# Kernel optimization log

Hardware: AMD Instinct MI355X
Metric: run time of the kernel (lower is better)

Reference implementation:

```python
import jax, jax.numpy as jnp
import numpy as np

B, Q, DIN, DOUT = 1, 1024, 4096, 4096
H, G, HD = 32, 8, 128          # heads, kv groups, head_dim; group_size = H // G
PREV = 3072                     # cached KV length
MAXPOS = 4096                   # rope table length (>= PREV + Q)
START = PREV


def _rope_tables(max_pos, head_dim):
    half = head_dim // 2
    inv_freq = 1.0 / (10000.0 ** (jnp.arange(half, dtype=jnp.float32) / half))
    ang = jnp.arange(max_pos, dtype=jnp.float32)[:, None] * inv_freq[None, :]
    ang = jnp.concatenate([ang, ang], axis=-1)  # [max_pos, head_dim]
    return jnp.cos(ang), jnp.sin(ang)


def apply_rope(x, cos, sin, start_pos):
    # x: [b, h, s, d]; rotate-half RoPE with absolute positions start_pos..start_pos+s
    s, d = x.shape[2], x.shape[3]
    c = cos[start_pos:start_pos + s]  # [s, d] (start_pos is a Python int)
    sn = sin[start_pos:start_pos + s]
    x1, x2 = x[..., : d // 2], x[..., d // 2:]
    rotated = jnp.concatenate([-x2, x1], axis=-1)
    return x * c + rotated * sn


def setup_inputs() -> dict:
    key = jax.random.key(0)
    ks = jax.random.split(key, 7)
    x = jax.random.normal(ks[0], (B, Q, DIN), dtype=jnp.float32)
    cos, sin = _rope_tables(MAXPOS, HD)
    # causal mask: query at abs position START+i may attend kv position j <= START+i
    qpos = START + jnp.arange(Q)
    kpos = jnp.arange(START + Q)
    mask = (kpos[None, :] > qpos[:, None])[None, None]  # [1,1,Q,KV], True = masked
    prev_k = jax.random.normal(ks[1], (B, G, PREV, HD), dtype=jnp.float32)
    prev_v = jax.random.normal(ks[2], (B, G, PREV, HD), dtype=jnp.float32)
    sc = 0.02
    Wq = jax.random.normal(ks[3], (DIN, DOUT), dtype=jnp.float32) * sc
    Wk = jax.random.normal(ks[4], (DIN, G * HD), dtype=jnp.float32) * sc
    Wv = jax.random.normal(ks[5], (DIN, G * HD), dtype=jnp.float32) * sc
    Wo = jax.random.normal(ks[6], (DOUT, DOUT), dtype=jnp.float32) * sc
    return dict(x=x, mask=mask, cos=cos, sin=sin, start_pos=START,
                prev_k=prev_k, prev_v=prev_v, Wq=Wq, Wk=Wk, Wv=Wv, Wo=Wo)


def reference(x, mask, cos, sin, start_pos, prev_k, prev_v, Wq, Wk, Wv, Wo):
    b, s, _ = x.shape
    gs = H // G  # group_size
    q = (x @ Wq).reshape(b, s, H, HD).transpose(0, 2, 1, 3)   # [b,H,s,hd]
    k = (x @ Wk).reshape(b, s, G, HD).transpose(0, 2, 1, 3)   # [b,G,s,hd]
    v = (x @ Wv).reshape(b, s, G, HD).transpose(0, 2, 1, 3)
    q = apply_rope(q, cos, sin, start_pos)
    k = apply_rope(k, cos, sin, start_pos)
    keys = jnp.concatenate([prev_k, k], axis=2)    # [b,G,KV,hd]
    values = jnp.concatenate([prev_v, v], axis=2)
    # grouped attention (equivalent to repeat_interleave of K/V over group_size)
    qg = q.reshape(b, G, gs, s, HD)
    scores = jnp.einsum('bgnqd,bgkd->bgnqk', qg, keys)        # [b,G,gs,s,KV]
    scores = jnp.where(mask[:, :, None], -jnp.inf, scores)
    attn = jax.nn.softmax(scores / np.sqrt(HD).astype(np.float32), axis=-1)
    ctx = jnp.einsum('bgnqk,bgkd->bgnqd', attn, values)       # [b,G,gs,s,hd]
    ctx = ctx.reshape(b, H, s, HD).transpose(0, 2, 1, 3).reshape(b, s, DOUT)
    out = ctx @ Wo
    return (out, keys, values)
```

## Files before the change

kernel.cpp:

```cpp
#include <hip/hip_runtime.h>
#include <hip/hip_bf16.h>

typedef unsigned short u16;
typedef unsigned int u32;
typedef __attribute__((ext_vector_type(4))) float f32x4;
typedef __attribute__((ext_vector_type(16))) float f32x16;
typedef __attribute__((ext_vector_type(8))) __bf16 bf16x8;
typedef __attribute__((ext_vector_type(4))) u16 u16x4;
typedef __attribute__((ext_vector_type(8))) u16 u16x8;
typedef __attribute__((ext_vector_type(4))) u32 u32x4;

#define START_POS 3072
#define NKV 4096
#define HD_ 128
#define SEQ 1024
#define DIN_ 4096
#define DQKV 6144

__device__ __forceinline__ void gll16(const void* g, void* l) {
  __builtin_amdgcn_global_load_lds((const __attribute__((address_space(1))) u32*)g,
                                   (__attribute__((address_space(3))) u32*)l, 16, 0, 0);
}
__device__ __forceinline__ u16 f2bf(float f) {
  u32 u = __builtin_bit_cast(u32, f);
  return (u16)((u + 0x7fffu + ((u >> 16) & 1u)) >> 16);
}
__device__ __forceinline__ u32 pack2bf(float a, float b) {
  __hip_bfloat162 t = __float22bfloat162_rn(float2{a, b});
  u32 u; __builtin_memcpy(&u, &t, 4);
  return u;
}
__device__ __forceinline__ f32x4 mfma16(bf16x8 a, bf16x8 b, f32x4 c) {
  return __builtin_amdgcn_mfma_f32_16x16x32_bf16(a, b, c, 0, 0, 0);
}
__device__ __forceinline__ f32x16 mfma32(bf16x8 a, bf16x8 b, f32x16 c) {
  return __builtin_amdgcn_mfma_f32_32x32x16_bf16(a, b, c, 0, 0, 0);
}

__global__ __launch_bounds__(256) void wtrans(const float* __restrict__ W,
    u16* __restrict__ Wt, int N, int ntn, int row_off)
{
  __shared__ float T[64][68];
  int bid = blockIdx.x;
  int nt = bid % ntn, kt = bid / ntn;
  int t = threadIdx.x;
  int kl = t >> 4, nl4 = (t & 15) << 2;
#pragma unroll
  for (int r = 0; r < 4; r++) {
    int row = r * 16 + kl;
    f32x4 v = *(const f32x4*)(W + (size_t)(kt * 64 + row) * N + nt * 64 + nl4);
    T[row][nl4] = v[0]; T[row][nl4 + 1] = v[1]; T[row][nl4 + 2] = v[2]; T[row][nl4 + 3] = v[3];
  }
  __syncthreads();
  int nl = t >> 2, k0 = (t & 3) << 4;
  u16x8 lo, hi;
#pragma unroll
  for (int j = 0; j < 8; j++) lo[j] = f2bf(T[k0 + j][nl]);
#pragma unroll
  for (int j = 0; j < 8; j++) hi[j] = f2bf(T[k0 + 8 + j][nl]);
  u16* dst = Wt + (size_t)(row_off + nt * 64 + nl) * 4096 + kt * 64 + k0;
  *(u16x8*)dst = lo;
  *(u16x8*)(dst + 8) = hi;
}

__global__ __launch_bounds__(256) void cvt_bf16(const float* __restrict__ src,
    u16* __restrict__ dst, int n4)
{
  int i = blockIdx.x * 256 + threadIdx.x;
  if (i >= n4) return;
  f32x4 v = *(const f32x4*)(src + (size_t)i * 4);
  u16x4 o;
#pragma unroll
  for (int j = 0; j < 4; j++) o[j] = f2bf(v[j]);
  *(u16x4*)(dst + (size_t)i * 4) = o;
}

__global__ __launch_bounds__(256) void gemm_bt(
    const u16* __restrict__ A, const u16* __restrict__ Bt,
    float* __restrict__ C, int N, int K, int nbx)
{
  __shared__ u16 As[2 * 128 * 32];
  __shared__ u16 Bs[2 * 64 * 32];
  int nwg = (int)gridDim.x;
  int orig = blockIdx.x;
  int q8 = nwg >> 3, r8 = nwg & 7;
  int xcd = orig & 7, jj = orig >> 3;
  int wgid = (xcd < r8 ? xcd * (q8 + 1) : r8 * (q8 + 1) + (xcd - r8) * q8) + jj;
  int by = wgid / nbx, bx = wgid % nbx;
  int tid = threadIdx.x, lane = tid & 63, wid = tid >> 6;
  int wr = wid >> 1, wc = wid & 1;
  int c = lane & 15, hh = lane >> 4;
  int lrow = wid * 16 + (lane >> 2);
  int ksl = (lane & 3) << 3;
  const u16* aS0 = A + (size_t)(by * 128 + lrow) * K + ksl;
  const u16* bS0 = Bt + (size_t)(bx * 64 + lrow) * K + ksl;

#define GSTAGE(buf, kk) do { \
  gll16(aS0 + (kk), As + (buf) * 4096 + wid * 512); \
  gll16(aS0 + (size_t)64 * K + (kk), As + (buf) * 4096 + 2048 + wid * 512); \
  gll16(bS0 + (kk), Bs + (buf) * 2048 + wid * 512); \
} while (0)

  f32x4 acc[4][2] = {};
  int nk = K >> 5;
  int cur = 0;
  GSTAGE(0, 0);
  __syncthreads();
  for (int kt = 0; kt < nk; kt++) {
    if (kt + 1 < nk) GSTAGE(cur ^ 1, (kt + 1) * 32);
    const u16* Ab = As + cur * 4096;
    const u16* Bb = Bs + cur * 2048;
    bf16x8 af[4], bf[2];
#pragma unroll
    for (int i = 0; i < 4; i++)
      af[i] = *(const bf16x8*)(Ab + (wr * 64 + i * 16 + c) * 32 + hh * 8);
#pragma unroll
    for (int i = 0; i < 2; i++)
      bf[i] = *(const bf16x8*)(Bb + (wc * 32 + i * 16 + c) * 32 + hh * 8);
    __builtin_amdgcn_s_setprio(1);
#pragma unroll
    for (int mi = 0; mi < 4; mi++)
#pragma unroll
      for (int ni = 0; ni < 2; ni++)
        acc[mi][ni] = mfma16(af[mi], bf[ni], acc[mi][ni]);
    __builtin_amdgcn_s_setprio(0);
    __syncthreads();
    cur ^= 1;
  }
#undef GSTAGE
  int row0 = by * 128 + wr * 64 + hh * 4;
  int col0 = bx * 64 + wc * 32 + c;
#pragma unroll
  for (int mi = 0; mi < 4; mi++)
#pragma unroll
    for (int ni = 0; ni < 2; ni++)
#pragma unroll
      for (int i = 0; i < 4; i++)
        C[(size_t)(row0 + mi * 16 + i) * N + col0 + ni * 16] = acc[mi][ni][i];
}

__global__ __launch_bounds__(256) void rope_q(const float* __restrict__ qkv,
    const float* __restrict__ cosb, const float* __restrict__ sinb, u16* __restrict__ qb)
{
  int tid = blockIdx.x * 256 + threadIdx.x;
  int dq = tid & 15, h = (tid >> 4) & 31, s = tid >> 9;
  int d = dq << 2;
  const float* base = qkv + (size_t)s * DQKV + h * HD_ + d;
  f32x4 a = *(const f32x4*)base;
  f32x4 b2 = *(const f32x4*)(base + 64);
  f32x4 cc = *(const f32x4*)(cosb + (size_t)(START_POS + s) * HD_ + d);
  f32x4 sn = *(const f32x4*)(sinb + (size_t)(START_POS + s) * HD_ + d);
  u16x4 o1, o2;
#pragma unroll
  for (int i = 0; i < 4; i++) {
    o1[i] = f2bf(a[i] * cc[i] - b2[i] * sn[i]);
    o2[i] = f2bf(b2[i] * cc[i] + a[i] * sn[i]);
  }
  u16* dst = qb + ((size_t)h * SEQ + s) * HD_ + d;
  *(u16x4*)dst = o1;
  *(u16x4*)(dst + 64) = o2;
}

__global__ __launch_bounds__(256) void rope_k(const float* __restrict__ qkv,
    const float* __restrict__ cosb, const float* __restrict__ sinb,
    float* __restrict__ keys, u16* __restrict__ kbb)
{
  int tid = blockIdx.x * 256 + threadIdx.x;
  int dq = tid & 15, g = (tid >> 4) & 7, s = tid >> 7;
  int d = dq << 2;
  const float* base = qkv + (size_t)s * DQKV + DIN_ + g * HD_ + d;
  f32x4 a = *(const f32x4*)base;
  f32x4 b2 = *(const f32x4*)(base + 64);
  f32x4 cc = *(const f32x4*)(cosb + (size_t)(START_POS + s) * HD_ + d);
  f32x4 sn = *(const f32x4*)(sinb + (size_t)(START_POS + s) * HD_ + d);
  f32x4 o1, o2;
  u16x4 p1, p2;
#pragma unroll
  for (int i = 0; i < 4; i++) {
    o1[i] = a[i] * cc[i] - b2[i] * sn[i];
    o2[i] = b2[i] * cc[i] + a[i] * sn[i];
    p1[i] = f2bf(o1[i]);
    p2[i] = f2bf(o2[i]);
  }
  size_t off = ((size_t)g * NKV + START_POS + s) * HD_ + d;
  *(f32x4*)(keys + off) = o1;
  *(f32x4*)(keys + off + 64) = o2;
  *(u16x4*)(kbb + off) = p1;
  *(u16x4*)(kbb + off + 64) = p2;
}

__global__ __launch_bounds__(256) void copy_vnew(const float* __restrict__ qkv,
    float* __restrict__ values)
{
  int tid = blockIdx.x * 256 + threadIdx.x;
  int dq = tid & 31, g = (tid >> 5) & 7, s = tid >> 8;
  int d = dq << 2;
  f32x4 v = *(const f32x4*)(qkv + (size_t)s * DQKV + DIN_ + 1024 + g * HD_ + d);
  *(f32x4*)(values + ((size_t)g * NKV + START_POS + s) * HD_ + d) = v;
}

__global__ __launch_bounds__(256) void prev_copy(const float* __restrict__ pk,
    const float* __restrict__ pv, float* __restrict__ keys, float* __restrict__ values,
    u16* __restrict__ kbb)
{
  int idx = blockIdx.x * 256 + threadIdx.x;
  int d4 = idx & 31;
  int rest = idx >> 5;
  int p = rest % 3072, g = rest / 3072;
  f32x4 kq = *(const f32x4*)(pk + (size_t)idx * 4);
  f32x4 vq = *(const f32x4*)(pv + (size_t)idx * 4);
  size_t off = ((size_t)g * NKV + p) * HD_ + d4 * 4;
  *(f32x4*)(keys + off) = kq;
  *(f32x4*)(values + off) = vq;
  u16x4 kb4;
#pragma unroll
  for (int i = 0; i < 4; i++) kb4[i] = f2bf(kq[i]);
  *(u16x4*)(kbb + off) = kb4;
}

__global__ __launch_bounds__(256) void vtrans(const float* __restrict__ pv,
    const float* __restrict__ qkv, u16* __restrict__ vT)
{
  __shared__ float T[64][68];
  int bid = blockIdx.x;
  int dt = bid & 1, pt = (bid >> 1) & 63, g = bid >> 7;
  int t = threadIdx.x;
  int pl = t >> 4, dl4 = (t & 15) << 2;
#pragma unroll
  for (int r = 0; r < 4; r++) {
    int row = r * 16 + pl;
    int pos = pt * 64 + row;
    f32x4 v;
    if (pos < START_POS)
      v = *(const f32x4*)(pv + ((size_t)g * START_POS + pos) * HD_ + dt * 64 + dl4);
    else
      v = *(const f32x4*)(qkv + (size_t)(pos - START_POS) * DQKV + 5120 + g * HD_ + dt * 64 + dl4);
    T[row][dl4] = v[0]; T[row][dl4 + 1] = v[1]; T[row][dl4 + 2] = v[2]; T[row][dl4 + 3] = v[3];
  }
  __syncthreads();
  int dl = t >> 2, p0 = (t & 3) << 4;
  u16x8 lo, hi;
#pragma unroll
  for (int j = 0; j < 8; j++) lo[j] = f2bf(T[p0 + j][dl]);
#pragma unroll
  for (int j = 0; j < 8; j++) hi[j] = f2bf(T[p0 + 8 + j][dl]);
  u16* dst = vT + ((size_t)g * HD_ + dt * 64 + dl) * NKV + pt * 64 + p0;
  *(u16x8*)dst = lo;
  *(u16x8*)(dst + 8) = hi;
}

__global__ __launch_bounds__(128, 2) void attn_fwd(
    const u16* __restrict__ qb, const u16* __restrict__ kb,
    const u16* __restrict__ vT, float* __restrict__ Opart, float* __restrict__ Ml)
{
  __shared__ u16 Ks[2 * 32 * 128];
  __shared__ u16 Vs[2 * 128 * 32];
  const float C2 = 0.12751744f;
  int bid = blockIdx.x;
  int g = bid & 7, j = bid >> 3;
  int sp = j >> 6, jj = j & 63;
  int h = g * 4 + (jj >> 4), qt = jj & 15;
  int tid = threadIdx.x, lane = tid & 63, w = tid >> 6;
  int c32 = lane & 31, h8 = lane >> 5;
  int qw0 = qt * 64 + w * 32;
  bf16x8 Qf[8];
#pragma unroll
  for (int dc = 0; dc < 8; dc++)
    Qf[dc] = *(const bf16x8*)(qb + ((size_t)(h * 1024 + qw0 + c32)) * 128 + dc * 16 + h8 * 8);
  f32x16 O0 = {}, O1 = {}, O2 = {}, O3 = {};
  float Mx = -1e30f, Ls = 0.f;
  int t0 = sp ? (49 + qt) : 0;
  int t1 = sp ? (98 + 2 * qt) : (49 + qt);

#define STAGE_KV(tt, bo) do { \
  _Pragma("unroll") \
  for (int r = 0; r < 4; r++) { \
    int s = w * 256 + r * 64 + lane; \
    int krow = s >> 4, sl = s & 15; \
    gll16(kb + ((size_t)(g * 4096 + (tt) * 32 + krow)) * 128 + (sl ^ (krow & 7)) * 8, \
          Ks + (bo) + (w * 256 + r * 64) * 8); \
    int d = s >> 2, sl2 = s & 3; \
    gll16(vT + ((size_t)(g * 128 + d)) * 4096 + (tt) * 32 + (sl2 ^ ((d >> 1) & 3)) * 8, \
          Vs + (bo) + (w * 256 + r * 64) * 8); \
  } \
} while (0)

  int cur = 0;
  STAGE_KV(t0, 0);
  __syncthreads();
  int vxr = (c32 >> 1) & 3;
  for (int t = t0; t < t1; t++) {
    if (t + 1 < t1) STAGE_KV(t + 1, (cur ^ 1) * 4096);
    const u16* Kb = Ks + cur * 4096;
    const u16* Vb = Vs + cur * 4096;
    f32x16 S0 = {}, Sb = {};
    __builtin_amdgcn_s_setprio(1);
#pragma unroll
    for (int dc = 0; dc < 8; dc += 2) {
      int sxA = (2 * dc + h8) ^ (c32 & 7);
      int sxB = (2 * dc + 2 + h8) ^ (c32 & 7);
      bf16x8 kA = *(const bf16x8*)(Kb + (size_t)c32 * 128 + sxA * 8);
      bf16x8 kB = *(const bf16x8*)(Kb + (size_t)c32 * 128 + sxB * 8);
      S0 = mfma32(kA, Qf[dc], S0);
      Sb = mfma32(kB, Qf[dc + 1], Sb);
    }
    __builtin_amdgcn_s_setprio(0);
#pragma unroll
    for (int r = 0; r < 16; r++) S0[r] += Sb[r];
    if (t * 32 + 31 > START_POS + qw0) {
      int qa = START_POS + qw0 + c32;
#pragma unroll
      for (int r = 0; r < 16; r++) {
        int kvo = t * 32 + (r & 3) + 8 * (r >> 2) + 4 * h8;
        if (kvo > qa) S0[r] = -1e30f;
      }
    }
    float tm[16];
#pragma unroll
    for (int r = 0; r < 16; r++) tm[r] = S0[r];
#pragma unroll
    for (int sft = 8; sft >= 1; sft >>= 1)
#pragma unroll
      for (int r = 0; r < sft; r++) tm[r] = fmaxf(tm[r], tm[r + sft]);
    float full = fmaxf(tm[0], __shfl_xor(tm[0], 32));
    if (!__all(full <= Mx + 62.0f)) {
      float Mn = fmaxf(Mx, full);
      float al = exp2f((Mx - Mn) * C2);
      Mx = Mn;
      Ls *= al;
#pragma unroll
      for (int r = 0; r < 16; r++) { O0[r] *= al; O1[r] *= al; O2[r] *= al; O3[r] *= al; }
    }
#pragma unroll
    for (int r = 0; r < 16; r++) S0[r] = exp2f((S0[r] - Mx) * C2);
    float ts[16];
#pragma unroll
    for (int r = 0; r < 16; r++) ts[r] = S0[r];
#pragma unroll
    for (int sft = 8; sft >= 1; sft >>= 1)
#pragma unroll
      for (int r = 0; r < sft; r++) ts[r] = ts[r] + ts[r + sft];
    Ls += ts[0] + __shfl_xor(ts[0], 32);
    u32 pk0[8], x0[8];
#pragma unroll
    for (int m = 0; m < 8; m++) pk0[m] = pack2bf(S0[2 * m], S0[2 * m + 1]);
#pragma unroll
    for (int m = 0; m < 8; m++) x0[m] = __shfl_xor(pk0[m], 32);
    bf16x8 pbf[2];
    {
      u32x4 f0 = { h8 ? x0[2] : pk0[0], h8 ? x0[3] : pk0[1],
                   h8 ? pk0[2] : x0[0], h8 ? pk0[3] : x0[1] };
      u32x4 f1 = { h8 ? x0[6] : pk0[4], h8 ? x0[7] : pk0[5],
                   h8 ? pk0[6] : x0[4], h8 ? pk0[7] : x0[5] };
      pbf[0] = __builtin_bit_cast(bf16x8, f0);
      pbf[1] = __builtin_bit_cast(bf16x8, f1);
    }
    __builtin_amdgcn_s_setprio(1);
#pragma unroll
    for (int kc = 0; kc < 2; kc++) {
      int sv = 2 * kc + h8;
      int sx = (sv ^ vxr) * 8;
      {
        bf16x8 vf = *(const bf16x8*)(Vb + (size_t)(0 * 32 + c32) * 32 + sx);
        O0 = mfma32(vf, pbf[kc], O0);
      }
      {
        bf16x8 vf = *(const bf16x8*)(Vb + (size_t)(1 * 32 + c32) * 32 + sx);
        O1 = mfma32(vf, pbf[kc], O1);
      }
      {
        bf16x8 vf = *(const bf16x8*)(Vb + (size_t)(2 * 32 + c32) * 32 + sx);
        O2 = mfma32(vf, pbf[kc], O2);
      }
      {
        bf16x8 vf = *(const bf16x8*)(Vb + (size_t)(3 * 32 + c32) * 32 + sx);
        O3 = mfma32(vf, pbf[kc], O3);
      }
    }
    __builtin_amdgcn_s_setprio(0);
    __syncthreads();
    cur ^= 1;
  }
#undef STAGE_KV
  {
    float* Orow = Opart + (size_t)sp * 4194304 + (size_t)(qw0 + c32) * 4096 + h * 128;
#pragma unroll
    for (int a = 0; a < 4; a++) {
      f32x4 o0, o1, o2, o3;
#pragma unroll
      for (int b = 0; b < 4; b++) {
        o0[b] = O0[4 * a + b]; o1[b] = O1[4 * a + b];
        o2[b] = O2[4 * a + b]; o3[b] = O3[4 * a + b];
      }
      int d0 = 8 * a + 4 * h8;
      *(f32x4*)(Orow + d0) = o0;
      *(f32x4*)(Orow + 32 + d0) = o1;
      *(f32x4*)(Orow + 64 + d0) = o2;
      *(f32x4*)(Orow + 96 + d0) = o3;
    }
    if (h8 == 0) {
      float* mp = Ml + ((size_t)(sp * 32 + h) * 1024 + qw0 + c32) * 2;
      mp[0] = Mx; mp[1] = Ls;
    }
  }
}

__global__ __launch_bounds__(256) void attn_combine(const float* __restrict__ Opart,
    const float* __restrict__ Ml, u16* __restrict__ ctxb)
{
  int idx = blockIdx.x * 256 + threadIdx.x;
  int q = idx >> 10, c4 = idx & 1023;
  int col = c4 * 4, h = col >> 7;
  const float* m0p = Ml + ((size_t)h * 1024 + q) * 2;
  const float* m1p = Ml + ((size_t)(32 + h) * 1024 + q) * 2;
  float m0 = m0p[0], l0 = m0p[1];
  float m1 = m1p[0], l1 = m1p[1];
  float M = fmaxf(m0, m1);
  float w0 = exp2f((m0 - M) * 0.12751744f);
  float w1 = exp2f((m1 - M) * 0.12751744f);
  float inv = 1.0f / (l0 * w0 + l1 * w1);
  f32x4 a = *(const f32x4*)(Opart + (size_t)q * 4096 + col);
  f32x4 b = *(const f32x4*)(Opart + 4194304 + (size_t)q * 4096 + col);
  u16x4 o;
#pragma unroll
  for (int i = 0; i < 4; i++) o[i] = f2bf((a[i] * w0 + b[i] * w1) * inv);
  *(u16x4*)(ctxb + (size_t)q * 4096 + col) = o;
}

extern "C" void kernel_launch(void* const* d_in, const int* in_sizes, int n_in,
                              void* d_out, int out_size, void* d_ws, size_t ws_size,
                              hipStream_t stream) {
  const float* x      = (const float*)d_in[0];
  const float* cosb   = (const float*)d_in[2];
  const float* sinb   = (const float*)d_in[3];
  const float* prev_k = (const float*)d_in[5];
  const float* prev_v = (const float*)d_in[6];
  const float* Wq     = (const float*)d_in[7];
  const float* Wk     = (const float*)d_in[8];
  const float* Wv     = (const float*)d_in[9];
  const float* Wo     = (const float*)d_in[10];

  u16* Wt_proj = (u16*)d_ws;
  u16* Wt_out  = Wt_proj + (size_t)6144 * 4096;
  u16* xb      = Wt_out + (size_t)4096 * 4096;
  float* qkv   = (float*)(xb + (size_t)1024 * 4096);
  u16* qb      = (u16*)(qkv + (size_t)1024 * 6144);
  u16* kbb     = qb + (size_t)32 * 1024 * 128;
  u16* vT      = kbb + (size_t)8 * 4096 * 128;
  u16* ctxb    = vT + (size_t)8 * 4096 * 128;
  float* Opart = (float*)d_ws;
  float* Ml    = Opart + (size_t)2 * 1024 * 4096;

  float* outp   = (float*)d_out;
  float* keys   = outp + (size_t)4194304;
  float* values = outp + (size_t)8388608;

  wtrans<<<4096, 256, 0, stream>>>(Wq, Wt_proj, 4096, 64, 0);
  wtrans<<<1024, 256, 0, stream>>>(Wk, Wt_proj, 1024, 16, 4096);
  wtrans<<<1024, 256, 0, stream>>>(Wv, Wt_proj, 1024, 16, 5120);
  wtrans<<<4096, 256, 0, stream>>>(Wo, Wt_out, 4096, 64, 0);
  cvt_bf16<<<4096, 256, 0, stream>>>(x, xb, 1048576);

  gemm_bt<<<768, 256, 0, stream>>>(xb, Wt_proj, qkv, 6144, 4096, 96);

  rope_q<<<2048, 256, 0, stream>>>(qkv, cosb, sinb, qb);
  rope_k<<<512, 256, 0, stream>>>(qkv, cosb, sinb, keys, kbb);
  copy_vnew<<<1024, 256, 0, stream>>>(qkv, values);
  prev_copy<<<3072, 256, 0, stream>>>(prev_k, prev_v, keys, values, kbb);
  vtrans<<<1024, 256, 0, stream>>>(prev_v, qkv, vT);

  attn_fwd<<<1024, 128, 0, stream>>>(qb, kbb, vT, Opart, Ml);
  attn_combine<<<4096, 256, 0, stream>>>(Opart, Ml, ctxb);

  gemm_bt<<<512, 256, 0, stream>>>(ctxb, Wt_out, outp, 4096, 4096, 64);
}
```

Baseline: 379.2 us.

## Split attention KV range three ways with single-buffered V staging and prescaled Q

The attention kernel now splits each query tile's KV range into three equal parts instead of two uneven ones, launching 1536 blocks. The combine kernel merges three partials, and the M/l buffer moves into the freed xb region. The softmax scale is folded into Q during RoPE so the inner loop drops a multiply per element. V is single-buffered in LDS with explicit vmcnt waits and barriers, so the V load overlaps the QK step and LDS use shrinks, at the cost of extra barriers. The rescale threshold is adjusted to the new log2 domain.

Result: slower. 398.3 us (+5.0%).

```diff
diff --git a/kernel.cpp b/kernel.cpp
--- a/kernel.cpp
+++ b/kernel.cpp
@@ -142,6 +142,7 @@
 __global__ __launch_bounds__(256) void rope_q(const float* __restrict__ qkv,
     const float* __restrict__ cosb, const float* __restrict__ sinb, u16* __restrict__ qb)
 {
+  const float C2 = 0.12751744f;
   int tid = blockIdx.x * 256 + threadIdx.x;
   int dq = tid & 15, h = (tid >> 4) & 31, s = tid >> 9;
   int d = dq << 2;
@@ -153,8 +154,8 @@
   u16x4 o1, o2;
 #pragma unroll
   for (int i = 0; i < 4; i++) {
-    o1[i] = f2bf(a[i] * cc[i] - b2[i] * sn[i]);
-    o2[i] = f2bf(b2[i] * cc[i] + a[i] * sn[i]);
+    o1[i] = f2bf((a[i] * cc[i] - b2[i] * sn[i]) * C2);
+    o2[i] = f2bf((b2[i] * cc[i] + a[i] * sn[i]) * C2);
   }
   u16* dst = qb + ((size_t)h * SEQ + s) * HD_ + d;
   *(u16x4*)dst = o1;
@@ -254,8 +255,7 @@
     const u16* __restrict__ vT, float* __restrict__ Opart, float* __restrict__ Ml)
 {
   __shared__ u16 Ks[2 * 32 * 128];
-  __shared__ u16 Vs[2 * 128 * 32];
-  const float C2 = 0.12751744f;
+  __shared__ u16 Vs[128 * 32];
   int bid = blockIdx.x;
   int g = bid & 7, j = bid >> 3;
   int sp = j >> 6, jj = j & 63;
@@ -269,30 +269,49 @@
     Qf[dc] = *(const bf16x8*)(qb + ((size_t)(h * 1024 + qw0 + c32)) * 128 + dc * 16 + h8 * 8);
   f32x16 O0 = {}, O1 = {}, O2 = {}, O3 = {};
   float Mx = -1e30f, Ls = 0.f;
-  int t0 = sp ? (49 + qt) : 0;
-  int t1 = sp ? (98 + 2 * qt) : (49 + qt);
-
-#define STAGE_KV(tt, bo) do { \
+  int T = 98 + 2 * qt;
+  int t0 = (sp * T) / 3;
+  int t1 = ((sp + 1) * T) / 3;
+
+#define STAGE_K(tt, bo) do { \
+  _Pragma("unroll") \
+  for (int r = 0; r < 2; r++) { \
+    int s = w * 256 + r * 128 + (lane & 63) + (lane >> 6) * 0; \
+    int s2 = w * 256 + r * 128 + lane; \
+    (void)s; \
+    int krow = s2 >> 4, sl = s2 & 15; \
+    gll16(kb + ((size_t)(g * 4096 + (tt) * 32 + krow)) * 128 + (sl ^ (krow & 7)) * 8, \
+          Ks + (bo) + (w * 256 + r * 128) * 8); \
+    int s3 = w * 256 + r * 128 + 64 + lane; \
+    int krow2 = s3 >> 4, sl2_ = s3 & 15; \
+    gll16(kb + ((size_t)(g * 4096 + (tt) * 32 + krow2)) * 128 + (sl2_ ^ (krow2 & 7)) * 8, \
+          Ks + (bo) + (w * 256 + r * 128 + 64) * 8); \
+  } \
+} while (0)
+
+#define STAGE_V(tt) do { \
   _Pragma("unroll") \
   for (int r = 0; r < 4; r++) { \
     int s = w * 256 + r * 64 + lane; \
-    int krow = s >> 4, sl = s & 15; \
-    gll16(kb + ((size_t)(g * 4096 + (tt) * 32 + krow)) * 128 + (sl ^ (krow & 7)) * 8, \
-          Ks + (bo) + (w * 256 + r * 64) * 8); \
     int d = s >> 2, sl2 = s & 3; \
     gll16(vT + ((size_t)(g * 128 + d)) * 4096 + (tt) * 32 + (sl2 ^ ((d >> 1) & 3)) * 8, \
-          Vs + (bo) + (w * 256 + r * 64) * 8); \
+          Vs + (w * 256 + r * 64) * 8); \
   } \
 } while (0)
 
   int cur = 0;
-  STAGE_KV(t0, 0);
-  __syncthreads();
+  STAGE_K(t0, 0);
   int vxr = (c32 >> 1) & 3;
   for (int t = t0; t < t1; t++) {
-    if (t + 1 < t1) STAGE_KV(t + 1, (cur ^ 1) * 4096);
+    bool last = (t + 1 >= t1);
+    STAGE_V(t);
+    if (!last) STAGE_K(t + 1, (cur ^ 1) * 4096);
+    if (!last) { asm volatile("s_waitcnt vmcnt(8)" ::: "memory"); }
+    else       { asm volatile("s_waitcnt vmcnt(4)" ::: "memory"); }
+    __builtin_amdgcn_sched_barrier(0);
+    __builtin_amdgcn_s_barrier();
+    __builtin_amdgcn_sched_barrier(0);
     const u16* Kb = Ks + cur * 4096;
-    const u16* Vb = Vs + cur * 4096;
     f32x16 S0 = {}, Sb = {};
     __builtin_amdgcn_s_setprio(1);
 #pragma unroll
@@ -323,16 +342,16 @@
 #pragma unroll
       for (int r = 0; r < sft; r++) tm[r] = fmaxf(tm[r], tm[r + sft]);
     float full = fmaxf(tm[0], __shfl_xor(tm[0], 32));
-    if (!__all(full <= Mx + 62.0f)) {
+    if (!__all(full <= Mx + 8.0f)) {
       float Mn = fmaxf(Mx, full);
-      float al = exp2f((Mx - Mn) * C2);
+      float al = exp2f(Mx - Mn);
       Mx = Mn;
       Ls *= al;
 #pragma unroll
       for (int r = 0; r < 16; r++) { O0[r] *= al; O1[r] *= al; O2[r] *= al; O3[r] *= al; }
     }
 #pragma unroll
-    for (int r = 0; r < 16; r++) S0[r] = exp2f((S0[r] - Mx) * C2);
+    for (int r = 0; r < 16; r++) S0[r] = exp2f(S0[r] - Mx);
     float ts[16];
 #pragma unroll
     for (int r = 0; r < 16; r++) ts[r] = S0[r];
@@ -355,33 +374,41 @@
       pbf[0] = __builtin_bit_cast(bf16x8, f0);
       pbf[1] = __builtin_bit_cast(bf16x8, f1);
     }
+    if (!last) { asm volatile("s_waitcnt vmcnt(4)" ::: "memory"); }
+    else       { asm volatile("s_waitcnt vmcnt(0)" ::: "memory"); }
+    __builtin_amdgcn_sched_barrier(0);
+    __builtin_amdgcn_s_barrier();
+    __builtin_amdgcn_sched_barrier(0);
     __builtin_amdgcn_s_setprio(1);
 #pragma unroll
     for (int kc = 0; kc < 2; kc++) {
       int sv = 2 * kc + h8;
       int sx = (sv ^ vxr) * 8;
       {
-        bf16x8 vf = *(const bf16x8*)(Vb + (size_t)(0 * 32 + c32) * 32 + sx);
+        bf16x8 vf = *(const bf16x8*)(Vs + (size_t)(0 * 32 + c32) * 32 + sx);
         O0 = mfma32(vf, pbf[kc], O0);
       }
       {
-        bf16x8 vf = *(const bf16x8*)(Vb + (size_t)(1 * 32 + c32) * 32 + sx);
+        bf16x8 vf = *(const bf16x8*)(Vs + (size_t)(1 * 32 + c32) * 32 + sx);
         O1 = mfma32(vf, pbf[kc], O1);
       }
       {
-        bf16x8 vf = *(const bf16x8*)(Vb + (size_t)(2 * 32 + c32) * 32 + sx);
+        bf16x8 vf = *(const bf16x8*)(Vs + (size_t)(2 * 32 + c32) * 32 + sx);
         O2 = mfma32(vf, pbf[kc], O2);
       }
       {
-        bf16x8 vf = *(const bf16x8*)(Vb + (size_t)(3 * 32 + c32) * 32 + sx);
+        bf16x8 vf = *(const bf16x8*)(Vs + (size_t)(3 * 32 + c32) * 32 + sx);
         O3 = mfma32(vf, pbf[kc], O3);
       }
     }
     __builtin_amdgcn_s_setprio(0);
-    __syncthreads();
+    __builtin_amdgcn_sched_barrier(0);
+    __builtin_amdgcn_s_barrier();
+    __builtin_amdgcn_sched_barrier(0);
     cur ^= 1;
   }
-#undef STAGE_KV
+#undef STAGE_K
+#undef STAGE_V
   {
     float* Orow = Opart + (size_t)sp * 4194304 + (size_t)(qw0 + c32) * 4096 + h * 128;
 #pragma unroll
@@ -413,17 +440,20 @@
   int col = c4 * 4, h = col >> 7;
   const float* m0p = Ml + ((size_t)h * 1024 + q) * 2;
   const float* m1p = Ml + ((size_t)(32 + h) * 1024 + q) * 2;
+  const float* m2p = Ml + ((size_t)(64 + h) * 1024 + q) * 2;
   float m0 = m0p[0], l0 = m0p[1];
   float m1 = m1p[0], l1 = m1p[1];
-  float M = fmaxf(m0, m1);
-  float w0 = exp2f((m0 - M) * 0.12751744f);
-  float w1 = exp2f((m1 - M) * 0.12751744f);
-  float inv = 1.0f / (l0 * w0 + l1 * w1);
+  float m2 = m2p[0], l2 = m2p[1];
+  float M = fmaxf(fmaxf(m0, m1), m2);
+  float w0 = exp2f(m0 - M), w1 = exp2f(m1 - M), w2 = exp2f(m2 - M);
+  float inv = 1.0f / (l0 * w0 + l1 * w1 + l2 * w2);
   f32x4 a = *(const f32x4*)(Opart + (size_t)q * 4096 + col);
   f32x4 b = *(const f32x4*)(Opart + 4194304 + (size_t)q * 4096 + col);
+  f32x4 cc = *(const f32x4*)(Opart + 2 * 4194304 + (size_t)q * 4096 + col);
   u16x4 o;
 #pragma unroll
-  for (int i = 0; i < 4; i++) o[i] = f2bf((a[i] * w0 + b[i] * w1) * inv);
+  for (int i = 0; i < 4; i++)
+    o[i] = f2bf((a[i] * w0 + b[i] * w1 + cc[i] * w2) * inv);
   *(u16x4*)(ctxb + (size_t)q * 4096 + col) = o;
 }
 
@@ -449,7 +479,7 @@
   u16* vT      = kbb + (size_t)8 * 4096 * 128;
   u16* ctxb    = vT + (size_t)8 * 4096 * 128;
   float* Opart = (float*)d_ws;
-  float* Ml    = Opart + (size_t)2 * 1024 * 4096;
+  float* Ml    = (float*)xb;
 
   float* outp   = (float*)d_out;
   float* keys   = outp + (size_t)4194304;
@@ -469,7 +499,7 @@
   prev_copy<<<3072, 256, 0, stream>>>(prev_k, prev_v, keys, values, kbb);
   vtrans<<<1024, 256, 0, stream>>>(prev_v, qkv, vT);
 
-  attn_fwd<<<1024, 128, 0, stream>>>(qb, kbb, vT, Opart, Ml);
+  attn_fwd<<<1536, 128, 0, stream>>>(qb, kbb, vT, Opart, Ml);
   attn_combine<<<4096, 256, 0, stream>>>(Opart, Ml, ctxb);
 
   gemm_bt<<<512, 256, 0, stream>>>(ctxb, Wt_out, outp, 4096, 4096, 64);
```
